# Performance work log

Measured on AMD Instinct MI355X. Metric: run time of the kernel, lower is better.

Reference implementation:

```python
import jax, jax.numpy as jnp
import numpy as np

B, V = 4, 10242
N = B * V            # 40968 packed vertices
E_PER = 30720        # edges per mesh
HID = 128


def _bilinear_sample(fm, grid):
    """pytorch3d vert_align core: grid_sample(align_corners=True, bilinear).
    fm: [B,C,H,W], grid: [B,V,2] xy in [-1,1] -> [B,V,C]."""
    b_, c_, h_, w_ = fm.shape
    x = (grid[..., 0] + 1.0) * 0.5 * (w_ - 1)
    y = (grid[..., 1] + 1.0) * 0.5 * (h_ - 1)
    x0f, y0f = jnp.floor(x), jnp.floor(y)
    wx1, wy1 = x - x0f, y - y0f
    wx0, wy0 = 1.0 - wx1, 1.0 - wy1
    x0 = jnp.clip(x0f, 0, w_ - 1).astype(jnp.int32)
    x1 = jnp.clip(x0f + 1, 0, w_ - 1).astype(jnp.int32)
    y0 = jnp.clip(y0f, 0, h_ - 1).astype(jnp.int32)
    y1 = jnp.clip(y0f + 1, 0, h_ - 1).astype(jnp.int32)
    fmt = jnp.transpose(fm, (0, 2, 3, 1))  # [B,H,W,C]
    bi = jnp.arange(b_)[:, None]
    g = lambda yy, xx: fmt[bi, yy, xx]     # [B,V,C]
    return ((wy0 * wx0)[..., None] * g(y0, x0)
            + (wy0 * wx1)[..., None] * g(y0, x1)
            + (wy1 * wx0)[..., None] * g(y1, x0)
            + (wy1 * wx1)[..., None] * g(y1, x1))


def _graph_conv(x, edges, w0, b0, w1, b1):
    """pytorch3d GraphConv (undirected): W0 x_i + sum over both edge dirs of W1 x_j."""
    h0 = x @ w0 + b0
    h1 = x @ w1 + b1
    e0, e1 = edges[:, 0], edges[:, 1]
    agg = jnp.zeros_like(h0).at[e0].add(h1[e1]).at[e1].add(h1[e0])
    return h0 + agg


def setup_inputs() -> dict:
    key = jax.random.key(0)
    ks = jax.random.split(key, 20)
    s = 0.05
    # per-mesh edges, offset into packed index space
    e = jax.random.randint(ks[0], (B, E_PER, 2), 0, V)
    e = e + (jnp.arange(B) * V)[:, None, None]
    return {
        "feat1": jax.random.normal(ks[1], (B, 256, 56, 56), jnp.float32),
        "feat2": jax.random.normal(ks[2], (B, 512, 28, 28), jnp.float32),
        "feat3": jax.random.normal(ks[3], (B, 1024, 14, 14), jnp.float32),
        "feat4": jax.random.normal(ks[4], (B, 2048, 7, 7), jnp.float32),
        "aligned_verts": jax.random.uniform(ks[5], (B, V, 3), jnp.float32, -1.0, 1.0),
        "verts_packed": jax.random.normal(ks[6], (N, 3), jnp.float32),
        "image_enc": jax.random.normal(ks[7], (B, 256), jnp.float32),
        "edges": e.reshape(B * E_PER, 2).astype(jnp.int64),
        "bottleneck_w": jax.random.normal(ks[8], (3840, HID), jnp.float32) * s,
        "bottleneck_b": jnp.zeros((HID,), jnp.float32),
        "g0_w0": jax.random.normal(ks[9], (387, HID), jnp.float32) * s,
        "g0_b0": jnp.zeros((HID,), jnp.float32),
        "g0_w1": jax.random.normal(ks[10], (387, HID), jnp.float32) * s,
        "g0_b1": jnp.zeros((HID,), jnp.float32),
        "gw0": jax.random.normal(ks[11], (7, HID, HID), jnp.float32) * s,
        "gb0": jnp.zeros((7, HID), jnp.float32),
        "gw1": jax.random.normal(ks[12], (7, HID, HID), jnp.float32) * s,
        "gb1": jnp.zeros((7, HID), jnp.float32),
        "off_w": jax.random.normal(ks[13], (HID, 3), jnp.float32) * s,
        "off_b": jnp.zeros((3,), jnp.float32),
    }


def reference(feat1, feat2, feat3, feat4, aligned_verts, verts_packed, image_enc,
              edges, bottleneck_w, bottleneck_b, g0_w0, g0_b0, g0_w1, g0_b1,
              gw0, gb0, gw1, gb1, off_w, off_b):
    grid = aligned_verts[..., :2]  # vert_align uses xy only
    samp = jnp.concatenate([_bilinear_sample(f, grid)
                            for f in (feat1, feat2, feat3, feat4)], axis=-1)
    samp = samp.reshape(N, 3840)  # return_packed=True
    vfeat = jax.nn.relu(samp @ bottleneck_w + bottleneck_b)
    enc = jnp.repeat(image_enc, V, axis=0)  # repeat_interleave
    x = jnp.concatenate([vfeat, verts_packed, enc], axis=1)  # [N,387]
    x = jax.nn.relu(_graph_conv(x, edges, g0_w0, g0_b0, g0_w1, g0_b1))
    for i in range(7):
        x = jax.nn.relu(_graph_conv(x, edges, gw0[i], gb0[i], gw1[i], gb1[i]))
    return x @ off_w + off_b  # delta_v [N,3]
```

## Files before the change

### kernel.cpp

```cpp
#include <hip/hip_runtime.h>

static inline int ceil_div(int a, int b) { return (a + b - 1) / b; }

typedef __attribute__((ext_vector_type(8))) short short8;
typedef __attribute__((ext_vector_type(4))) float floatx4;

__device__ __forceinline__ unsigned short f2bf(float f) {
    unsigned int u = __float_as_uint(f);
    unsigned int r = (u + 0x7fffu + ((u >> 16) & 1u)) >> 16;
    return (unsigned short)r;
}
__device__ __forceinline__ float bf2f(unsigned short h) {
    return __uint_as_float(((unsigned int)h) << 16);
}

__global__ __launch_bounds__(1024) void scan1_k(const int* __restrict__ deg,
                                                int* __restrict__ excl,
                                                int* __restrict__ bsum, int Nv) {
    __shared__ int s[1024];
    int tid = threadIdx.x;
    int i = blockIdx.x * 1024 + tid;
    int v = (i < Nv) ? deg[i] : 0;
    s[tid] = v;
    __syncthreads();
    for (int off = 1; off < 1024; off <<= 1) {
        int t = (tid >= off) ? s[tid - off] : 0;
        __syncthreads();
        if (tid >= off) s[tid] += t;
        __syncthreads();
    }
    if (i < Nv) excl[i] = s[tid] - v;
    if (tid == 1023) bsum[blockIdx.x] = s[1023];
}

__global__ __launch_bounds__(1024) void scan3_k(const int* __restrict__ excl,
                                                const int* __restrict__ bsum,
                                                const int* __restrict__ deg,
                                                int* __restrict__ rowptr,
                                                int* __restrict__ cursor, int Nv, int nb) {
    __shared__ int offS;
    if (threadIdx.x < 64) {
        int v = (threadIdx.x < min((int)blockIdx.x, nb)) ? bsum[threadIdx.x] : 0;
#pragma unroll
        for (int m = 1; m < 64; m <<= 1) v += __shfl_xor(v, m);
        if (threadIdx.x == 0) offS = v;
    }
    __syncthreads();
    int i = blockIdx.x * 1024 + threadIdx.x;
    if (i < Nv) {
        int val = excl[i] + offS;
        rowptr[i] = val;
        cursor[i] = val;
        if (i == Nv - 1) rowptr[Nv] = val + deg[i];
    }
}

__global__ __launch_bounds__(256) void fill_adj_k(const int* __restrict__ edges,
                                                  int* __restrict__ cursor,
                                                  int* __restrict__ adj, int E) {
    int e = blockIdx.x * blockDim.x + threadIdx.x;
    if (e < E) {
        int a = edges[2 * e], b = edges[2 * e + 1];
        adj[atomicAdd(&cursor[a], 1)] = b;
        adj[atomicAdd(&cursor[b], 1)] = a;
    }
}

__global__ __launch_bounds__(256) void fatpre_k(const int* __restrict__ edges,
                                                int* __restrict__ deg, int E, int nE,
                                                const float* __restrict__ g0w0,
                                                const float* __restrict__ g0w1,
                                                const float* __restrict__ gw0,
                                                const float* __restrict__ gw1,
                                                unsigned short* __restrict__ Wt,
                                                const float* __restrict__ bw,
                                                unsigned short* __restrict__ bwT,
                                                const float* __restrict__ enc,
                                                float* __restrict__ encp, int B_) {
    int bid = blockIdx.x;
    int tid = threadIdx.x;
    if (bid < nE) {
        int e = bid * 256 + tid;
        if (e < E) {
            atomicAdd(&deg[edges[2 * e]], 1);
            atomicAdd(&deg[edges[2 * e + 1]], 1);
        }
    } else if (bid < nE + 16) {
        int lh = bid - nE;
        int l = lh >> 1, h = lh & 1;
        const float* src;
        if (l == 0) src = h ? g0w1 : g0w0;
        else src = (h ? gw1 : gw0) + (size_t)(l - 1) * 16384;
        unsigned short* dst = Wt + (size_t)lh * 16384;
        for (int idx = tid; idx < 16384; idx += 256) {
            int n = idx >> 7, k = idx & 127;
            dst[n * 128 + k] = f2bf(src[k * 128 + n]);
        }
    } else if (bid < nE + 46) {
        int blk = bid - nE - 16;
        for (int idx = tid; idx < 16384; idx += 256) {
            int n = idx >> 7, kk = idx & 127;
            bwT[(size_t)n * 3840 + blk * 128 + kk] =
                f2bf(bw[(size_t)(blk * 128 + kk) * 128 + n]);
        }
    } else {
        int b = bid - nE - 46;
        int sH = tid >> 7;
        int j = tid & 127;
        const float* w = sH ? g0w1 : g0w0;
        const float* eb = enc + b * 256;
        float acc = 0.f;
        for (int c = 0; c < 256; ++c) acc = fmaf(eb[c], w[(131 + c) * 128 + j], acc);
        encp[(sH * B_ + b) * 128 + j] = acc;
    }
}

__global__ __launch_bounds__(256) void proj_all_k(
    const float* __restrict__ fm1, const float* __restrict__ fm2,
    const float* __restrict__ fm3, const float* __restrict__ fm4,
    const unsigned short* __restrict__ bwT, float* __restrict__ o1, float* __restrict__ o2,
    float* __restrict__ o3, float* __restrict__ o4, int B_) {
    __shared__ unsigned short wlds[8192];

    int tid = threadIdx.x;
    int n1 = 49 * B_ * 2, n2 = 13 * B_ * 4, n3 = 4 * B_ * 8;
    int bid = blockIdx.x;
    const float* fm;
    float* op;
    int C, HW, PT, idx, koff;
    if (bid < n1) {
        fm = fm1; op = o1; C = 256; HW = 3136; PT = 49; idx = bid; koff = 0;
    } else if (bid < n1 + n2) {
        fm = fm2; op = o2; C = 512; HW = 784; PT = 13; idx = bid - n1; koff = 256;
    } else if (bid < n1 + n2 + n3) {
        fm = fm3; op = o3; C = 1024; HW = 196; PT = 4; idx = bid - n1 - n2; koff = 768;
    } else {
        fm = fm4; op = o4; C = 2048; HW = 49; PT = 1; idx = bid - n1 - n2 - n3; koff = 1792;
    }
    int pt = idx % PT;
    int r2 = idx / PT;
    int b = r2 % B_;
    int zz = r2 / B_;
    int p0 = pt * 64;
    const float* fmb = fm + (size_t)b * C * HW;
    int kcf0 = zz * 128;

    int wave = tid >> 6, lane = tid & 63;
    int row16 = lane & 15, quad = lane >> 4;
    int p = p0 + wave * 16 + row16;
    bool pok = (p < HW);
    int pc = pok ? p : 0;

    floatx4 acc[8];
#pragma unroll
    for (int j = 0; j < 8; ++j) acc[j] = (floatx4){0.f, 0.f, 0.f, 0.f};

#pragma unroll
    for (int zz2 = 0; zz2 < 2; ++zz2) {
        int kcf = kcf0 + zz2 * 64;
        int kcw = koff + kcf;
        if (zz2) __syncthreads();
#pragma unroll
        for (int l = 0; l < 4; ++l) {
            int i2 = tid + l * 256;
            int n = i2 >> 3, c16 = i2 & 7;
            *(short8*)&wlds[n * 64 + ((c16 ^ (n & 7)) * 8)] =
                *(const short8*)(bwT + (size_t)n * 3840 + kcw + c16 * 8);
        }
        short8 ax[2];
#pragma unroll
        for (int ks = 0; ks < 2; ++ks) {
#pragma unroll
            for (int j = 0; j < 8; ++j) {
                float v = pok ? fmb[(size_t)(kcf + ks * 32 + quad * 8 + j) * HW + pc] : 0.f;
                ax[ks][j] = (short)f2bf(v);
            }
        }
        __syncthreads();
#pragma unroll
        for (int ks = 0; ks < 2; ++ks) {
            int c = ks * 4 + quad;
#pragma unroll
            for (int nt = 0; nt < 8; ++nt) {
                int wr = nt * 16 + row16;
                short8 bwf = *(short8*)&wlds[wr * 64 + ((c ^ (wr & 7)) * 8)];
                acc[nt] =
                    __builtin_amdgcn_mfma_f32_16x16x32_bf16(ax[ks], bwf, acc[nt], 0, 0, 0);
            }
        }
    }

    float* obase = op + (size_t)b * HW * 128;
#pragma unroll
    for (int nt = 0; nt < 8; ++nt) {
        int colg = nt * 16 + row16;
#pragma unroll
        for (int rr = 0; rr < 4; ++rr) {
            int pr = p0 + wave * 16 + quad * 4 + rr;
            if (pr < HW) atomicAdd(&obase[(size_t)pr * 128 + colg], acc[nt][rr]);
        }
    }
}

__device__ __forceinline__ float sample_level(const float* __restrict__ pp, int Hh, int Ww,
                                              float gx, float gy, int j) {
    float x = (gx + 1.f) * 0.5f * (float)(Ww - 1);
    float y = (gy + 1.f) * 0.5f * (float)(Hh - 1);
    float x0f = floorf(x), y0f = floorf(y);
    float wx1 = x - x0f, wy1 = y - y0f;
    float wx0 = 1.f - wx1, wy0 = 1.f - wy1;
    int x0 = (int)fminf(fmaxf(x0f, 0.f), (float)(Ww - 1));
    int x1 = (int)fminf(fmaxf(x0f + 1.f, 0.f), (float)(Ww - 1));
    int y0 = (int)fminf(fmaxf(y0f, 0.f), (float)(Hh - 1));
    int y1 = (int)fminf(fmaxf(y0f + 1.f, 0.f), (float)(Hh - 1));
    const float* r00 = pp + (size_t)(y0 * Ww + x0) * 128;
    const float* r01 = pp + (size_t)(y0 * Ww + x1) * 128;
    const float* r10 = pp + (size_t)(y1 * Ww + x0) * 128;
    const float* r11 = pp + (size_t)(y1 * Ww + x1) * 128;
    return wy0 * (wx0 * r00[j] + wx1 * r01[j]) + wy1 * (wx0 * r10[j] + wx1 * r11[j]);
}

__global__ __launch_bounds__(128) void sample_bottleneck_k(
    const float* __restrict__ av, const float* __restrict__ pp1, const float* __restrict__ pp2,
    const float* __restrict__ pp3, const float* __restrict__ pp4, const float* __restrict__ bb,
    const float* __restrict__ verts, const float* __restrict__ encp,
    const float* __restrict__ g0w0, const float* __restrict__ g0w1,
    const float* __restrict__ g0b0, const float* __restrict__ g0b1,
    unsigned short* __restrict__ X, unsigned short* __restrict__ H, int V_, int B_) {
    int n = blockIdx.x, j = threadIdx.x;
    int b = n / V_;
    float gx = av[(size_t)n * 3 + 0];
    float gy = av[(size_t)n * 3 + 1];
    float acc = bb[j];
    acc += sample_level(pp1 + (size_t)b * 3136 * 128, 56, 56, gx, gy, j);
    acc += sample_level(pp2 + (size_t)b * 784 * 128, 28, 28, gx, gy, j);
    acc += sample_level(pp3 + (size_t)b * 196 * 128, 14, 14, gx, gy, j);
    acc += sample_level(pp4 + (size_t)b * 49 * 128, 7, 7, gx, gy, j);
    X[(size_t)n * 128 + j] = f2bf(fmaxf(acc, 0.f));
    float v0 = verts[n * 3 + 0], v1 = verts[n * 3 + 1], v2 = verts[n * 3 + 2];
    float h0 = encp[(0 * B_ + b) * 128 + j] + g0b0[j] + v0 * g0w0[128 * 128 + j] +
               v1 * g0w0[129 * 128 + j] + v2 * g0w0[130 * 128 + j];
    float h1 = encp[(1 * B_ + b) * 128 + j] + g0b1[j] + v0 * g0w1[128 * 128 + j] +
               v1 * g0w1[129 * 128 + j] + v2 * g0w1[130 * 128 + j];
    H[(size_t)n * 256 + j] = f2bf(h0);
    H[(size_t)n * 256 + 128 + j] = f2bf(h1);
}

__global__ __launch_bounds__(256) void agg0_k(const unsigned short* __restrict__ X,
                                              const unsigned short* __restrict__ H,
                                              const int* __restrict__ rowptr,
                                              const int* __restrict__ adj,
                                              unsigned short* __restrict__ AggX,
                                              unsigned short* __restrict__ AggH, int Nv,
                                              int Etot) {
    int wave = threadIdx.x >> 6, lane = threadIdx.x & 63;
    int n0 = (blockIdx.x * 4 + wave) * 4;
    if (n0 >= Nv) return;
    int g = lane >> 4, c = lane & 15;
    int rp = rowptr[min(n0 + (lane & 7), Nv)];
    int sg = __shfl(rp, g);
    int eg = __shfl(rp, g + 1);
    int m = eg - sg;
    m = max(m, __shfl_xor(m, 16));
    m = max(m, __shfl_xor(m, 32));

    int n = n0 + g;
    bool nok = (n < Nv);
    int nc = nok ? n : (Nv - 1);
    float accx[8], acch[8];
    short8 h0v = *(const short8*)(H + (size_t)nc * 256 + c * 8);
#pragma unroll
    for (int j = 0; j < 8; ++j) {
        accx[j] = 0.f;
        acch[j] = bf2f((unsigned short)h0v[j]);
    }

    for (int it = 0; it < m; it += 8) {
        int t = sg + it + (lane & 7);
        int adjv = adj[min(t, Etot - 1)];
        short8 bx[8], bh[8];
#pragma unroll
        for (int q = 0; q < 8; ++q) {
            int nbq = __shfl(adjv, (lane & 48) + q);
            bx[q] = *(const short8*)(X + (size_t)nbq * 128 + c * 8);
            bh[q] = *(const short8*)(H + (size_t)nbq * 256 + 128 + c * 8);
        }
#pragma unroll
        for (int q = 0; q < 8; ++q) {
            bool ok = (sg + it + q < eg);
#pragma unroll
            for (int j = 0; j < 8; ++j) {
                accx[j] += ok ? bf2f((unsigned short)bx[q][j]) : 0.f;
                acch[j] += ok ? bf2f((unsigned short)bh[q][j]) : 0.f;
            }
        }
    }
    if (nok) {
        short8 ox, oh;
#pragma unroll
        for (int j = 0; j < 8; ++j) {
            ox[j] = (short)f2bf(accx[j]);
            oh[j] = (short)f2bf(acch[j]);
        }
        *(short8*)(AggX + (size_t)n * 128 + c * 8) = ox;
        *(short8*)(AggH + (size_t)n * 128 + c * 8) = oh;
    }
}

__global__ __launch_bounds__(256) void agg_x_k(const unsigned short* __restrict__ X,
                                               const int* __restrict__ rowptr,
                                               const int* __restrict__ adj,
                                               unsigned short* __restrict__ Agg, int Nv,
                                               int Etot) {
    int wave = threadIdx.x >> 6, lane = threadIdx.x & 63;
    int n0 = (blockIdx.x * 4 + wave) * 4;
    if (n0 >= Nv) return;
    int g = lane >> 4, c = lane & 15;
    int rp = rowptr[min(n0 + (lane & 7), Nv)];
    int sg = __shfl(rp, g);
    int eg = __shfl(rp, g + 1);
    int m = eg - sg;
    m = max(m, __shfl_xor(m, 16));
    m = max(m, __shfl_xor(m, 32));

    float acc[8];
#pragma unroll
    for (int j = 0; j < 8; ++j) acc[j] = 0.f;

    for (int it = 0; it < m; it += 8) {
        int t = sg + it + (lane & 7);
        int adjv = adj[min(t, Etot - 1)];
        short8 buf[8];
#pragma unroll
        for (int q = 0; q < 8; ++q) {
            int nbq = __shfl(adjv, (lane & 48) + q);
            buf[q] = *(const short8*)(X + (size_t)nbq * 128 + c * 8);
        }
#pragma unroll
        for (int q = 0; q < 8; ++q) {
            bool ok = (sg + it + q < eg);
#pragma unroll
            for (int j = 0; j < 8; ++j) {
                float v = bf2f((unsigned short)buf[q][j]);
                acc[j] += ok ? v : 0.f;
            }
        }
    }

    if (n0 + g < Nv) {
        short8 o;
#pragma unroll
        for (int j = 0; j < 8; ++j) o[j] = (short)f2bf(acc[j]);
        *(short8*)(Agg + (size_t)(n0 + g) * 128 + c * 8) = o;
    }
}

__global__ __launch_bounds__(256, 3) void gemm_dual_k(
    const unsigned short* __restrict__ Xin, const unsigned short* __restrict__ Agg,
    const unsigned short* __restrict__ Wt,
    const float* __restrict__ b0, const float* __restrict__ b1,
    const unsigned short* __restrict__ aggh, const int* __restrict__ degv,
    unsigned short* __restrict__ Xout, int M, const float* __restrict__ ow,
    const float* __restrict__ ob, float* __restrict__ outp) {
    __shared__ unsigned short wlds[16384];
    __shared__ unsigned short cs[64 * 72];
    __shared__ float bS[128];
    __shared__ float owS[192];

    int tid = threadIdx.x;
    int m0 = blockIdx.x * 128;
    int yb = blockIdx.y;

    int wave = tid >> 6, lane = tid & 63;
    int row16 = lane & 15;
    int quad = lane >> 4;
    int wrow = wave * 16;

    short8 axT[2][4], agT[2][4];
    int dgT[2][4];
    {
        int g = min(m0 + wrow + row16, M - 1);
#pragma unroll
        for (int ks = 0; ks < 4; ++ks) {
            int koff = ks * 32 + quad * 8;
            axT[0][ks] = *(const short8*)(Xin + (size_t)g * 128 + koff);
            agT[0][ks] = *(const short8*)(Agg + (size_t)g * 128 + koff);
        }
#pragma unroll
        for (int rr = 0; rr < 4; ++rr)
            dgT[0][rr] = degv[min(m0 + wrow + quad * 4 + rr, M - 1)];
    }

    if (tid < 64) {
        bS[tid] = b0 ? b0[yb * 64 + tid] : 0.f;
        bS[64 + tid] = b1 ? b1[yb * 64 + tid] : 0.f;
    }
    if (outp && tid < 192) owS[tid] = ow[yb * 192 + tid];

    const unsigned short* W0h = Wt + (size_t)yb * 64 * 128;
    const unsigned short* W1h = Wt + 16384 + (size_t)yb * 64 * 128;
#pragma unroll
    for (int l = 0; l < 8; ++l) {
        int idx = tid + l * 256;
        int half = idx >> 10;
        int r = (idx >> 4) & 63;
        int c16 = idx & 15;
        int sw = (c16 ^ (r & 15)) * 8;
        const unsigned short* src = (half ? W1h : W0h) + r * 128 + c16 * 8;
        *(short8*)&wlds[half * 8192 + r * 128 + sw] = *(const short8*)src;
    }
    __syncthreads();

    {
        int g = min(m0 + 64 + wrow + row16, M - 1);
#pragma unroll
        for (int ks = 0; ks < 4; ++ks) {
            int koff = ks * 32 + quad * 8;
            axT[1][ks] = *(const short8*)(Xin + (size_t)g * 128 + koff);
            agT[1][ks] = *(const short8*)(Agg + (size_t)g * 128 + koff);
        }
#pragma unroll
        for (int rr = 0; rr < 4; ++rr)
            dgT[1][rr] = degv[min(m0 + 64 + wrow + quad * 4 + rr, M - 1)];
    }

#pragma unroll
    for (int t = 0; t < 2; ++t) {
        int mT = m0 + t * 64;
        floatx4 acc[4];
#pragma unroll
        for (int j = 0; j < 4; j++) acc[j] = (floatx4){0.f, 0.f, 0.f, 0.f};

#pragma unroll
        for (int ks = 0; ks < 4; ++ks) {
            int c = ks * 4 + quad;
#pragma unroll
            for (int nt = 0; nt < 4; ++nt) {
                int wr = nt * 16 + row16;
                short8 bw0 = *(short8*)&wlds[wr * 128 + ((c ^ row16) * 8)];
                short8 bw1 = *(short8*)&wlds[8192 + wr * 128 + ((c ^ row16) * 8)];
                acc[nt] = __builtin_amdgcn_mfma_f32_16x16x32_bf16(axT[t][ks], bw0, acc[nt], 0, 0, 0);
                acc[nt] = __builtin_amdgcn_mfma_f32_16x16x32_bf16(agT[t][ks], bw1, acc[nt], 0, 0, 0);
            }
        }

        unsigned short cvs[4][4];
#pragma unroll
        for (int nt = 0; nt < 4; ++nt) {
            int colh = nt * 16 + row16;
            int colg = yb * 64 + colh;
            float bc0 = bS[colh];
            float bc1 = bS[64 + colh];
#pragma unroll
            for (int rr = 0; rr < 4; ++rr) {
                int row = wrow + quad * 4 + rr;
                int gm = mT + row;
                float v = acc[nt][rr] + bc0 + (float)dgT[t][rr] * bc1;
                if (aggh && gm < M) v += bf2f(aggh[(size_t)gm * 128 + colg]);
                unsigned short cv = f2bf(fmaxf(v, 0.f));
                cvs[nt][rr] = cv;
                cs[row * 72 + colh] = cv;
            }
        }

        if (outp) {
#pragma unroll
            for (int rr = 0; rr < 4; ++rr) {
                float h0 = 0.f, h1 = 0.f, h2 = 0.f;
#pragma unroll
                for (int nt = 0; nt < 4; ++nt) {
                    int colh = nt * 16 + row16;
                    float xv = bf2f(cvs[nt][rr]);
                    h0 += xv * owS[colh * 3 + 0];
                    h1 += xv * owS[colh * 3 + 1];
                    h2 += xv * owS[colh * 3 + 2];
                }
#pragma unroll
                for (int mm = 1; mm < 16; mm <<= 1) {
                    h0 += __shfl_xor(h0, mm);
                    h1 += __shfl_xor(h1, mm);
                    h2 += __shfl_xor(h2, mm);
                }
                if (row16 == 0) {
                    int gm = mT + wrow + quad * 4 + rr;
                    if (gm < M) {
                        float e0 = (yb == 0) ? ob[0] : 0.f;
                        float e1 = (yb == 0) ? ob[1] : 0.f;
                        float e2 = (yb == 0) ? ob[2] : 0.f;
                        atomicAdd(&outp[gm * 3 + 0], h0 + e0);
                        atomicAdd(&outp[gm * 3 + 1], h1 + e1);
                        atomicAdd(&outp[gm * 3 + 2], h2 + e2);
                    }
                }
            }
        }
        __syncthreads();

        {
            int r = tid >> 2;
            int cq = (tid & 3) * 16;
            int gm = mT + r;
            if (gm < M) {
                unsigned short* dst = Xout + (size_t)gm * 128 + yb * 64 + cq;
                *(short8*)dst = *(short8*)&cs[r * 72 + cq];
                *(short8*)(dst + 8) = *(short8*)&cs[r * 72 + cq + 8];
            }
        }
        __syncthreads();
    }
}

extern "C" void kernel_launch(void* const* d_in, const int* in_sizes, int n_in, void* d_out,
                              int out_size, void* d_ws, size_t ws_size, hipStream_t stream) {
    const float* feat1 = (const float*)d_in[0];
    const float* feat2 = (const float*)d_in[1];
    const float* feat3 = (const float*)d_in[2];
    const float* feat4 = (const float*)d_in[3];
    const float* av = (const float*)d_in[4];
    const float* verts = (const float*)d_in[5];
    const float* image_enc = (const float*)d_in[6];
    const int* edges = (const int*)d_in[7];
    const float* bw = (const float*)d_in[8];
    const float* bb = (const float*)d_in[9];
    const float* g0w0 = (const float*)d_in[10];
    const float* g0b0 = (const float*)d_in[11];
    const float* g0w1 = (const float*)d_in[12];
    const float* g0b1 = (const float*)d_in[13];
    const float* gw0 = (const float*)d_in[14];
    const float* gb0 = (const float*)d_in[15];
    const float* gw1 = (const float*)d_in[16];
    const float* gb1 = (const float*)d_in[17];
    const float* off_w = (const float*)d_in[18];
    const float* off_b = (const float*)d_in[19];

    int B_ = in_sizes[6] / 256;
    int N_ = in_sizes[5] / 3;
    int V_ = N_ / B_;
    int E_ = in_sizes[7] / 2;

    char* wsb = (char*)d_ws;
    size_t off = 0;
    auto alloc = [&](size_t bytes) -> void* {
        void* p = (void*)(wsb + off);
        off += (bytes + 255) & ~(size_t)255;
        return p;
    };
    int S1 = B_ * 3136 * 128;
    int S2 = B_ * 784 * 128;
    int S3 = B_ * 196 * 128;
    int S4 = B_ * 49 * 128;
    float* pp1 = (float*)alloc((size_t)S1 * 4);
    float* pp2 = (float*)alloc((size_t)S2 * 4);
    float* pp3 = (float*)alloc((size_t)S3 * 4);
    float* pp4 = (float*)alloc((size_t)S4 * 4);
    size_t pp_bytes = off;
    unsigned short* XA = (unsigned short*)alloc((size_t)N_ * 128 * 2);
    unsigned short* XB = (unsigned short*)alloc((size_t)N_ * 128 * 2);
    unsigned short* AggB = (unsigned short*)alloc((size_t)N_ * 128 * 2);
    unsigned short* AggH = (unsigned short*)alloc((size_t)N_ * 128 * 2);
    unsigned short* Hb = (unsigned short*)alloc((size_t)N_ * 256 * 2);
    unsigned short* Wt = (unsigned short*)alloc((size_t)8 * 2 * 128 * 128 * 2);
    unsigned short* bwT = (unsigned short*)alloc((size_t)128 * 3840 * 2);
    float* encp = (float*)alloc((size_t)2 * B_ * 128 * 4);
    int* deg = (int*)alloc((size_t)(N_ + 1) * 4);
    int* rowptr = (int*)alloc((size_t)(N_ + 1) * 4);
    int* cursor = (int*)alloc((size_t)N_ * 4);
    int* excl = (int*)alloc((size_t)N_ * 4);
    int* bsum = (int*)alloc((size_t)64 * 4);
    int* adj = (int*)alloc((size_t)2 * E_ * 4);

    hipMemsetAsync(deg, 0, (N_ + 1) * sizeof(int), stream);
    hipMemsetAsync(wsb, 0, pp_bytes, stream);
    hipMemsetAsync(d_out, 0, out_size, stream);

    int nE = ceil_div(E_, 256);
    fatpre_k<<<nE + 46 + B_, 256, 0, stream>>>(edges, deg, E_, nE, g0w0, g0w1, gw0, gw1, Wt,
                                               bw, bwT, image_enc, encp, B_);

    int nb = ceil_div(N_, 1024);
    scan1_k<<<nb, 1024, 0, stream>>>(deg, excl, bsum, N_);
    scan3_k<<<nb, 1024, 0, stream>>>(excl, bsum, deg, rowptr, cursor, N_, nb);
    fill_adj_k<<<ceil_div(E_, 256), 256, 0, stream>>>(edges, cursor, adj, E_);

    int nproj = 49 * B_ * 2 + 13 * B_ * 4 + 4 * B_ * 8 + 1 * B_ * 16;
    proj_all_k<<<nproj, 256, 0, stream>>>(feat1, feat2, feat3, feat4, bwT, pp1, pp2, pp3, pp4,
                                          B_);

    sample_bottleneck_k<<<N_, 128, 0, stream>>>(av, pp1, pp2, pp3, pp4, bb, verts, encp, g0w0,
                                                g0w1, g0b0, g0b1, XA, Hb, V_, B_);

    dim3 ggrid(ceil_div(N_, 128), 2);
    int agrid4 = ceil_div(N_, 16);
    agg0_k<<<agrid4, 256, 0, stream>>>(XA, Hb, rowptr, adj, AggB, AggH, N_, 2 * E_);
    gemm_dual_k<<<ggrid, 256, 0, stream>>>(XA, AggB, Wt, nullptr, nullptr, AggH, deg, XB, N_,
                                           nullptr, nullptr, nullptr);
    unsigned short* Xc = XB;
    unsigned short* Xn = XA;
    for (int i = 0; i < 7; ++i) {
        bool last = (i == 6);
        agg_x_k<<<agrid4, 256, 0, stream>>>(Xc, rowptr, adj, AggB, N_, 2 * E_);
        gemm_dual_k<<<ggrid, 256, 0, stream>>>(Xc, AggB, Wt + (size_t)(i + 1) * 32768,
                                               gb0 + i * 128, gb1 + i * 128, nullptr, deg, Xn,
                                               N_, last ? off_w : nullptr,
                                               last ? off_b : nullptr,
                                               last ? (float*)d_out : nullptr);
        unsigned short* t = Xc;
        Xc = Xn;
        Xn = t;
    }
}
```

Measured before the change: 431.4 us.

## Fuse neighbor aggregation and dual GEMM into one per-layer kernel

Replaces the separate agg_x_k gather kernel and gemm_dual_k launch for layers 1-7 with a single layer_fused_k. Each block gathers neighbor sums for 64 rows into LDS, then runs MFMA against weights read directly from global memory and writes the ReLU output. This removes the Agg buffer round trip through global memory and one launch per layer. The output projection is now computed over all 128 columns in one block, so plain stores replace the atomics and the output memset is dropped. Costs: weights are no longer staged in LDS, each block computes all 128 output columns, and register pressure rises with 8 accumulator tiles.

```diff
diff --git a/kernel.cpp b/kernel.cpp
--- a/kernel.cpp
+++ b/kernel.cpp
@@ -307,65 +307,15 @@
     }
 }
 
-__global__ __launch_bounds__(256) void agg_x_k(const unsigned short* __restrict__ X,
-                                               const int* __restrict__ rowptr,
-                                               const int* __restrict__ adj,
-                                               unsigned short* __restrict__ Agg, int Nv,
-                                               int Etot) {
-    int wave = threadIdx.x >> 6, lane = threadIdx.x & 63;
-    int n0 = (blockIdx.x * 4 + wave) * 4;
-    if (n0 >= Nv) return;
-    int g = lane >> 4, c = lane & 15;
-    int rp = rowptr[min(n0 + (lane & 7), Nv)];
-    int sg = __shfl(rp, g);
-    int eg = __shfl(rp, g + 1);
-    int m = eg - sg;
-    m = max(m, __shfl_xor(m, 16));
-    m = max(m, __shfl_xor(m, 32));
-
-    float acc[8];
-#pragma unroll
-    for (int j = 0; j < 8; ++j) acc[j] = 0.f;
-
-    for (int it = 0; it < m; it += 8) {
-        int t = sg + it + (lane & 7);
-        int adjv = adj[min(t, Etot - 1)];
-        short8 buf[8];
-#pragma unroll
-        for (int q = 0; q < 8; ++q) {
-            int nbq = __shfl(adjv, (lane & 48) + q);
-            buf[q] = *(const short8*)(X + (size_t)nbq * 128 + c * 8);
-        }
-#pragma unroll
-        for (int q = 0; q < 8; ++q) {
-            bool ok = (sg + it + q < eg);
-#pragma unroll
-            for (int j = 0; j < 8; ++j) {
-                float v = bf2f((unsigned short)buf[q][j]);
-                acc[j] += ok ? v : 0.f;
-            }
-        }
-    }
-
-    if (n0 + g < Nv) {
-        short8 o;
-#pragma unroll
-        for (int j = 0; j < 8; ++j) o[j] = (short)f2bf(acc[j]);
-        *(short8*)(Agg + (size_t)(n0 + g) * 128 + c * 8) = o;
-    }
-}
-
 __global__ __launch_bounds__(256, 3) void gemm_dual_k(
     const unsigned short* __restrict__ Xin, const unsigned short* __restrict__ Agg,
     const unsigned short* __restrict__ Wt,
     const float* __restrict__ b0, const float* __restrict__ b1,
     const unsigned short* __restrict__ aggh, const int* __restrict__ degv,
-    unsigned short* __restrict__ Xout, int M, const float* __restrict__ ow,
-    const float* __restrict__ ob, float* __restrict__ outp) {
+    unsigned short* __restrict__ Xout, int M) {
     __shared__ unsigned short wlds[16384];
     __shared__ unsigned short cs[64 * 72];
     __shared__ float bS[128];
-    __shared__ float owS[192];
 
     int tid = threadIdx.x;
     int m0 = blockIdx.x * 128;
@@ -395,7 +345,6 @@
         bS[tid] = b0 ? b0[yb * 64 + tid] : 0.f;
         bS[64 + tid] = b1 ? b1[yb * 64 + tid] : 0.f;
     }
-    if (outp && tid < 192) owS[tid] = ow[yb * 192 + tid];
 
     const unsigned short* W0h = Wt + (size_t)yb * 64 * 128;
     const unsigned short* W1h = Wt + 16384 + (size_t)yb * 64 * 128;
@@ -444,7 +393,6 @@
             }
         }
 
-        unsigned short cvs[4][4];
 #pragma unroll
         for (int nt = 0; nt < 4; ++nt) {
             int colh = nt * 16 + row16;
@@ -457,41 +405,7 @@
                 int gm = mT + row;
                 float v = acc[nt][rr] + bc0 + (float)dgT[t][rr] * bc1;
                 if (aggh && gm < M) v += bf2f(aggh[(size_t)gm * 128 + colg]);
-                unsigned short cv = f2bf(fmaxf(v, 0.f));
-                cvs[nt][rr] = cv;
-                cs[row * 72 + colh] = cv;
-            }
-        }
-
-        if (outp) {
-#pragma unroll
-            for (int rr = 0; rr < 4; ++rr) {
-                float h0 = 0.f, h1 = 0.f, h2 = 0.f;
-#pragma unroll
-                for (int nt = 0; nt < 4; ++nt) {
-                    int colh = nt * 16 + row16;
-                    float xv = bf2f(cvs[nt][rr]);
-                    h0 += xv * owS[colh * 3 + 0];
-                    h1 += xv * owS[colh * 3 + 1];
-                    h2 += xv * owS[colh * 3 + 2];
-                }
-#pragma unroll
-                for (int mm = 1; mm < 16; mm <<= 1) {
-                    h0 += __shfl_xor(h0, mm);
-                    h1 += __shfl_xor(h1, mm);
-                    h2 += __shfl_xor(h2, mm);
-                }
-                if (row16 == 0) {
-                    int gm = mT + wrow + quad * 4 + rr;
-                    if (gm < M) {
-                        float e0 = (yb == 0) ? ob[0] : 0.f;
-                        float e1 = (yb == 0) ? ob[1] : 0.f;
-                        float e2 = (yb == 0) ? ob[2] : 0.f;
-                        atomicAdd(&outp[gm * 3 + 0], h0 + e0);
-                        atomicAdd(&outp[gm * 3 + 1], h1 + e1);
-                        atomicAdd(&outp[gm * 3 + 2], h2 + e2);
-                    }
-                }
+                cs[row * 72 + colh] = f2bf(fmaxf(v, 0.f));
             }
         }
         __syncthreads();
@@ -507,6 +421,160 @@
             }
         }
         __syncthreads();
+    }
+}
+
+__global__ __launch_bounds__(256, 4) void layer_fused_k(
+    const unsigned short* __restrict__ Xin, const int* __restrict__ rowptr,
+    const int* __restrict__ adj, const unsigned short* __restrict__ Wt,
+    const float* __restrict__ b0, const float* __restrict__ b1,
+    const int* __restrict__ degv, unsigned short* __restrict__ Xout, int M, int Etot,
+    const float* __restrict__ ow, const float* __restrict__ ob,
+    float* __restrict__ outp) {
+    __shared__ unsigned short aggs[4096];
+    __shared__ unsigned short aggs2[4096];
+
+    int tid = threadIdx.x;
+    int m0 = blockIdx.x * 64;
+    int wave = tid >> 6, lane = tid & 63;
+    int row16 = lane & 15, quad = lane >> 4;
+    int wrow = wave * 16;
+    unsigned short* ag = (wave < 2) ? aggs : aggs2;
+    int wbase = (wave & 1) * 2048;
+
+    short8 axT[4];
+    {
+        int g = min(m0 + wrow + row16, M - 1);
+#pragma unroll
+        for (int ks = 0; ks < 4; ++ks)
+            axT[ks] = *(const short8*)(Xin + (size_t)g * 128 + ks * 32 + quad * 8);
+    }
+    int dgT[4];
+#pragma unroll
+    for (int rr = 0; rr < 4; ++rr)
+        dgT[rr] = degv[min(m0 + wrow + quad * 4 + rr, M - 1)];
+
+    int g16 = lane >> 4, c = lane & 15;
+#pragma unroll 1
+    for (int v = 0; v < 4; ++v) {
+        int base = m0 + wrow + v * 4;
+        int rp = rowptr[min(base + (lane & 7), M)];
+        int sg = __shfl(rp, g16);
+        int eg = __shfl(rp, g16 + 1);
+        int m = eg - sg;
+        m = max(m, __shfl_xor(m, 16));
+        m = max(m, __shfl_xor(m, 32));
+        float acc[8];
+#pragma unroll
+        for (int j = 0; j < 8; ++j) acc[j] = 0.f;
+        for (int it = 0; it < m; it += 8) {
+            int t = sg + it + (lane & 7);
+            int adjv = adj[min(t, Etot - 1)];
+            short8 buf[8];
+#pragma unroll
+            for (int q = 0; q < 8; ++q) {
+                int nbq = __shfl(adjv, (lane & 48) + q);
+                buf[q] = *(const short8*)(Xin + (size_t)nbq * 128 + c * 8);
+            }
+#pragma unroll
+            for (int q = 0; q < 8; ++q) {
+                bool ok = (sg + it + q < eg);
+#pragma unroll
+                for (int j = 0; j < 8; ++j)
+                    acc[j] += ok ? bf2f((unsigned short)buf[q][j]) : 0.f;
+            }
+        }
+        short8 o;
+#pragma unroll
+        for (int j = 0; j < 8; ++j) o[j] = (short)f2bf(acc[j]);
+        int rl = v * 4 + g16;
+        *(short8*)&ag[wbase + rl * 128 + ((c ^ rl) * 8)] = o;
+    }
+
+    floatx4 acc[8];
+#pragma unroll
+    for (int j = 0; j < 8; ++j) acc[j] = (floatx4){0.f, 0.f, 0.f, 0.f};
+#pragma unroll
+    for (int ks = 0; ks < 4; ++ks) {
+        int cc = ks * 4 + quad;
+        short8 agf = *(short8*)&ag[wbase + row16 * 128 + ((cc ^ row16) * 8)];
+#pragma unroll
+        for (int nt = 0; nt < 8; ++nt) {
+            int wr = nt * 16 + row16;
+            short8 bw0 = *(const short8*)(Wt + (size_t)wr * 128 + cc * 8);
+            short8 bw1 = *(const short8*)(Wt + 16384 + (size_t)wr * 128 + cc * 8);
+            acc[nt] = __builtin_amdgcn_mfma_f32_16x16x32_bf16(axT[ks], bw0, acc[nt], 0, 0, 0);
+            acc[nt] = __builtin_amdgcn_mfma_f32_16x16x32_bf16(agf, bw1, acc[nt], 0, 0, 0);
+        }
+    }
+
+    unsigned short cvs[8][4];
+#pragma unroll
+    for (int nt = 0; nt < 8; ++nt) {
+        int colh = nt * 16 + row16;
+        float bc0 = b0[colh];
+        float bc1 = b1[colh];
+#pragma unroll
+        for (int rr = 0; rr < 4; ++rr) {
+            float v = acc[nt][rr] + bc0 + (float)dgT[rr] * bc1;
+            cvs[nt][rr] = f2bf(fmaxf(v, 0.f));
+        }
+    }
+#pragma unroll
+    for (int nt = 0; nt < 8; ++nt) {
+        int colh = nt * 16 + row16;
+        int ch = colh >> 3;
+#pragma unroll
+        for (int rr = 0; rr < 4; ++rr) {
+            int rl = quad * 4 + rr;
+            ag[wbase + rl * 128 + ((ch ^ rl) * 8) + (colh & 7)] = cvs[nt][rr];
+        }
+    }
+
+    if (outp) {
+#pragma unroll
+        for (int rr = 0; rr < 4; ++rr) {
+            float h0 = 0.f, h1 = 0.f, h2 = 0.f;
+#pragma unroll
+            for (int nt = 0; nt < 8; ++nt) {
+                int colh = nt * 16 + row16;
+                float xv = bf2f(cvs[nt][rr]);
+                h0 += xv * ow[colh * 3 + 0];
+                h1 += xv * ow[colh * 3 + 1];
+                h2 += xv * ow[colh * 3 + 2];
+            }
+#pragma unroll
+            for (int mm = 1; mm < 16; mm <<= 1) {
+                h0 += __shfl_xor(h0, mm);
+                h1 += __shfl_xor(h1, mm);
+                h2 += __shfl_xor(h2, mm);
+            }
+            if (row16 == 0) {
+                int gm = m0 + wrow + quad * 4 + rr;
+                if (gm < M) {
+                    outp[gm * 3 + 0] = h0 + ob[0];
+                    outp[gm * 3 + 1] = h1 + ob[1];
+                    outp[gm * 3 + 2] = h2 + ob[2];
+                }
+            }
+        }
+    }
+    __syncthreads();
+
+    {
+        int r = tid >> 2;
+        int gm = m0 + r;
+        if (gm < M) {
+            unsigned short* src = (r < 32) ? aggs : aggs2;
+            int rb = (r & 31) >= 16 ? 2048 : 0;
+            int rl = r & 15;
+            unsigned short* dst = Xout + (size_t)gm * 128 + (tid & 3) * 32;
+#pragma unroll
+            for (int i = 0; i < 4; ++i) {
+                int ch = (tid & 3) * 4 + i;
+                *(short8*)(dst + i * 8) = *(short8*)&src[rb + rl * 128 + ((ch ^ rl) * 8)];
+            }
+        }
     }
 }
 
@@ -571,7 +639,6 @@
 
     hipMemsetAsync(deg, 0, (N_ + 1) * sizeof(int), stream);
     hipMemsetAsync(wsb, 0, pp_bytes, stream);
-    hipMemsetAsync(d_out, 0, out_size, stream);
 
     int nE = ceil_div(E_, 256);
     fatpre_k<<<nE + 46 + B_, 256, 0, stream>>>(edges, deg, E_, nE, g0w0, g0w1, gw0, gw1, Wt,
@@ -592,18 +659,17 @@
     dim3 ggrid(ceil_div(N_, 128), 2);
     int agrid4 = ceil_div(N_, 16);
     agg0_k<<<agrid4, 256, 0, stream>>>(XA, Hb, rowptr, adj, AggB, AggH, N_, 2 * E_);
-    gemm_dual_k<<<ggrid, 256, 0, stream>>>(XA, AggB, Wt, nullptr, nullptr, AggH, deg, XB, N_,
-                                           nullptr, nullptr, nullptr);
+    gemm_dual_k<<<ggrid, 256, 0, stream>>>(XA, AggB, Wt, nullptr, nullptr, AggH, deg, XB, N_);
+
     unsigned short* Xc = XB;
     unsigned short* Xn = XA;
+    int fgrid = ceil_div(N_, 64);
     for (int i = 0; i < 7; ++i) {
         bool last = (i == 6);
-        agg_x_k<<<agrid4, 256, 0, stream>>>(Xc, rowptr, adj, AggB, N_, 2 * E_);
-        gemm_dual_k<<<ggrid, 256, 0, stream>>>(Xc, AggB, Wt + (size_t)(i + 1) * 32768,
-                                               gb0 + i * 128, gb1 + i * 128, nullptr, deg, Xn,
-                                               N_, last ? off_w : nullptr,
-                                               last ? off_b : nullptr,
-                                               last ? (float*)d_out : nullptr);
+        layer_fused_k<<<fgrid, 256, 0, stream>>>(
+            Xc, rowptr, adj, Wt + (size_t)(i + 1) * 32768, gb0 + i * 128, gb1 + i * 128, deg,
+            Xn, N_, 2 * E_, last ? off_w : nullptr, last ? off_b : nullptr,
+            last ? (float*)d_out : nullptr);
         unsigned short* t = Xc;
         Xc = Xn;
         Xn = t;
```

Result: slower. 526.2 us (+22.0%).

## Pre-transpose feature maps to channel-last bf16 before projection GEMM

Applied to the files above, without the earlier changes.

Adds a tiled LDS transpose stage to the prep kernel that converts each NCHW fp32 feature map into a [B,HW,C] bf16 buffer. The projection kernel then loads its A fragments as contiguous 16-byte vector reads instead of eight strided scalar fp32 loads with per-element conversion. This adds an extra pass over the feature maps and extra workspace memory, but is meant to make the MFMA operand loads coalesced and cheaper. Out-of-range rows now clamp to the last valid pixel instead of zeroing, which is harmless only if those outputs are masked at store.

```diff
diff --git a/kernel.cpp b/kernel.cpp
--- a/kernel.cpp
+++ b/kernel.cpp
@@ -66,17 +66,17 @@
     }
 }
 
-__global__ __launch_bounds__(256) void fatpre_k(const int* __restrict__ edges,
-                                                int* __restrict__ deg, int E, int nE,
-                                                const float* __restrict__ g0w0,
-                                                const float* __restrict__ g0w1,
-                                                const float* __restrict__ gw0,
-                                                const float* __restrict__ gw1,
-                                                unsigned short* __restrict__ Wt,
-                                                const float* __restrict__ bw,
-                                                unsigned short* __restrict__ bwT,
-                                                const float* __restrict__ enc,
-                                                float* __restrict__ encp, int B_) {
+__global__ __launch_bounds__(256) void fatpre_k(
+    const int* __restrict__ edges, int* __restrict__ deg, int E, int nE,
+    const float* __restrict__ g0w0, const float* __restrict__ g0w1,
+    const float* __restrict__ gw0, const float* __restrict__ gw1,
+    unsigned short* __restrict__ Wt, const float* __restrict__ bw,
+    unsigned short* __restrict__ bwT, const float* __restrict__ enc,
+    float* __restrict__ encp, const float* __restrict__ fm1, const float* __restrict__ fm2,
+    const float* __restrict__ fm3, const float* __restrict__ fm4,
+    unsigned short* __restrict__ ft1, unsigned short* __restrict__ ft2,
+    unsigned short* __restrict__ ft3, unsigned short* __restrict__ ft4, int B_) {
+    __shared__ float tl[64][65];
     int bid = blockIdx.x;
     int tid = threadIdx.x;
     if (bid < nE) {
@@ -103,7 +103,7 @@
             bwT[(size_t)n * 3840 + blk * 128 + kk] =
                 f2bf(bw[(size_t)(blk * 128 + kk) * 128 + n]);
         }
-    } else {
+    } else if (bid < nE + 46 + B_) {
         int b = bid - nE - 46;
         int sH = tid >> 7;
         int j = tid & 127;
@@ -112,12 +112,67 @@
         float acc = 0.f;
         for (int c = 0; c < 256; ++c) acc = fmaf(eb[c], w[(131 + c) * 128 + j], acc);
         encp[(sH * B_ + b) * 128 + j] = acc;
+    } else {
+        int idx = bid - (nE + 46 + B_);
+        const float* fm;
+        unsigned short* ft;
+        int C, HW, PT, CT;
+        int q1 = 49 * 4 * B_, q2 = 13 * 8 * B_, q3 = 4 * 16 * B_;
+        if (idx < q1) {
+            fm = fm1; ft = ft1; C = 256; HW = 3136; PT = 49; CT = 4;
+        } else if ((idx -= q1) < q2) {
+            fm = fm2; ft = ft2; C = 512; HW = 784; PT = 13; CT = 8;
+        } else if ((idx -= q2) < q3) {
+            fm = fm3; ft = ft3; C = 1024; HW = 196; PT = 4; CT = 16;
+        } else {
+            idx -= q3;
+            fm = fm4; ft = ft4; C = 2048; HW = 49; PT = 1; CT = 32;
+        }
+        int ct = idx % CT;
+        int r2 = idx / CT;
+        int pt = r2 % PT;
+        int b = r2 / PT;
+        int p0 = pt * 64, c0 = ct * 64;
+        const float* fb = fm + (size_t)b * C * HW;
+#pragma unroll
+        for (int l = 0; l < 4; ++l) {
+            int i = tid + l * 256;
+            int ch = i >> 4;
+            int pq = (i & 15) * 4;
+            const float* src = fb + (size_t)(c0 + ch) * HW + p0 + pq;
+            float4 v;
+            if (p0 + pq + 3 < HW) {
+                v = *(const float4*)src;
+            } else {
+                v.x = (p0 + pq + 0 < HW) ? src[0] : 0.f;
+                v.y = (p0 + pq + 1 < HW) ? src[1] : 0.f;
+                v.z = (p0 + pq + 2 < HW) ? src[2] : 0.f;
+                v.w = (p0 + pq + 3 < HW) ? src[3] : 0.f;
+            }
+            tl[ch][pq + 0] = v.x;
+            tl[ch][pq + 1] = v.y;
+            tl[ch][pq + 2] = v.z;
+            tl[ch][pq + 3] = v.w;
+        }
+        __syncthreads();
+#pragma unroll
+        for (int l = 0; l < 2; ++l) {
+            int i = tid + l * 256;
+            int p = i >> 3;
+            int cc = (i & 7) * 8;
+            if (p0 + p < HW) {
+                short8 o;
+#pragma unroll
+                for (int j = 0; j < 8; ++j) o[j] = (short)f2bf(tl[cc + j][p]);
+                *(short8*)(ft + ((size_t)b * HW + p0 + p) * C + c0 + cc) = o;
+            }
+        }
     }
 }
 
 __global__ __launch_bounds__(256) void proj_all_k(
-    const float* __restrict__ fm1, const float* __restrict__ fm2,
-    const float* __restrict__ fm3, const float* __restrict__ fm4,
+    const unsigned short* __restrict__ ft1, const unsigned short* __restrict__ ft2,
+    const unsigned short* __restrict__ ft3, const unsigned short* __restrict__ ft4,
     const unsigned short* __restrict__ bwT, float* __restrict__ o1, float* __restrict__ o2,
     float* __restrict__ o3, float* __restrict__ o4, int B_) {
     __shared__ unsigned short wlds[8192];
@@ -125,31 +180,31 @@
     int tid = threadIdx.x;
     int n1 = 49 * B_ * 2, n2 = 13 * B_ * 4, n3 = 4 * B_ * 8;
     int bid = blockIdx.x;
-    const float* fm;
+    const unsigned short* ft;
     float* op;
     int C, HW, PT, idx, koff;
     if (bid < n1) {
-        fm = fm1; op = o1; C = 256; HW = 3136; PT = 49; idx = bid; koff = 0;
+        ft = ft1; op = o1; C = 256; HW = 3136; PT = 49; idx = bid; koff = 0;
     } else if (bid < n1 + n2) {
-        fm = fm2; op = o2; C = 512; HW = 784; PT = 13; idx = bid - n1; koff = 256;
+        ft = ft2; op = o2; C = 512; HW = 784; PT = 13; idx = bid - n1; koff = 256;
     } else if (bid < n1 + n2 + n3) {
-        fm = fm3; op = o3; C = 1024; HW = 196; PT = 4; idx = bid - n1 - n2; koff = 768;
+        ft = ft3; op = o3; C = 1024; HW = 196; PT = 4; idx = bid - n1 - n2; koff = 768;
     } else {
-        fm = fm4; op = o4; C = 2048; HW = 49; PT = 1; idx = bid - n1 - n2 - n3; koff = 1792;
+        ft = ft4; op = o4; C = 2048; HW = 49; PT = 1; idx = bid - n1 - n2 - n3; koff = 1792;
     }
     int pt = idx % PT;
     int r2 = idx / PT;
     int b = r2 % B_;
     int zz = r2 / B_;
     int p0 = pt * 64;
-    const float* fmb = fm + (size_t)b * C * HW;
     int kcf0 = zz * 128;
 
     int wave = tid >> 6, lane = tid & 63;
     int row16 = lane & 15, quad = lane >> 4;
     int p = p0 + wave * 16 + row16;
     bool pok = (p < HW);
-    int pc = pok ? p : 0;
+    int pc = pok ? p : (HW - 1);
+    const unsigned short* frow = ft + ((size_t)b * HW + pc) * C;
 
     floatx4 acc[8];
 #pragma unroll
@@ -169,13 +224,8 @@
         }
         short8 ax[2];
 #pragma unroll
-        for (int ks = 0; ks < 2; ++ks) {
-#pragma unroll
-            for (int j = 0; j < 8; ++j) {
-                float v = pok ? fmb[(size_t)(kcf + ks * 32 + quad * 8 + j) * HW + pc] : 0.f;
-                ax[ks][j] = (short)f2bf(v);
-            }
-        }
+        for (int ks = 0; ks < 2; ++ks)
+            ax[ks] = *(const short8*)(frow + kcf + ks * 32 + quad * 8);
         __syncthreads();
 #pragma unroll
         for (int ks = 0; ks < 2; ++ks) {
@@ -554,6 +604,10 @@
     float* pp3 = (float*)alloc((size_t)S3 * 4);
     float* pp4 = (float*)alloc((size_t)S4 * 4);
     size_t pp_bytes = off;
+    unsigned short* fmT1 = (unsigned short*)alloc((size_t)B_ * 3136 * 256 * 2);
+    unsigned short* fmT2 = (unsigned short*)alloc((size_t)B_ * 784 * 512 * 2);
+    unsigned short* fmT3 = (unsigned short*)alloc((size_t)B_ * 196 * 1024 * 2);
+    unsigned short* fmT4 = (unsigned short*)alloc((size_t)B_ * 49 * 2048 * 2);
     unsigned short* XA = (unsigned short*)alloc((size_t)N_ * 128 * 2);
     unsigned short* XB = (unsigned short*)alloc((size_t)N_ * 128 * 2);
     unsigned short* AggB = (unsigned short*)alloc((size_t)N_ * 128 * 2);
@@ -574,8 +628,10 @@
     hipMemsetAsync(d_out, 0, out_size, stream);
 
     int nE = ceil_div(E_, 256);
-    fatpre_k<<<nE + 46 + B_, 256, 0, stream>>>(edges, deg, E_, nE, g0w0, g0w1, gw0, gw1, Wt,
-                                               bw, bwT, image_enc, encp, B_);
+    int NT = (49 * 4 + 13 * 8 + 4 * 16 + 1 * 32) * B_;
+    fatpre_k<<<nE + 46 + B_ + NT, 256, 0, stream>>>(
+        edges, deg, E_, nE, g0w0, g0w1, gw0, gw1, Wt, bw, bwT, image_enc, encp, feat1, feat2,
+        feat3, feat4, fmT1, fmT2, fmT3, fmT4, B_);
 
     int nb = ceil_div(N_, 1024);
     scan1_k<<<nb, 1024, 0, stream>>>(deg, excl, bsum, N_);
@@ -583,7 +639,7 @@
     fill_adj_k<<<ceil_div(E_, 256), 256, 0, stream>>>(edges, cursor, adj, E_);
 
     int nproj = 49 * B_ * 2 + 13 * B_ * 4 + 4 * B_ * 8 + 1 * B_ * 16;
-    proj_all_k<<<nproj, 256, 0, stream>>>(feat1, feat2, feat3, feat4, bwT, pp1, pp2, pp3, pp4,
+    proj_all_k<<<nproj, 256, 0, stream>>>(fmT1, fmT2, fmT3, fmT4, bwT, pp1, pp2, pp3, pp4,
                                           B_);
 
     sample_bottleneck_k<<<N_, 128, 0, stream>>>(av, pp1, pp2, pp3, pp4, bb, verts, encp, g0w0,
```

Result: no change. 435.7 us (+1.0%).
